# Performance work log

Hardware: AMD Instinct MI355X
Metric: run time of the kernel (lower is better)

## Reference

```python
import jax, jax.numpy as jnp
import numpy as np

D_MODEL = 1024
N_HEADS = 16
D_EXP = 4
B, SQ, SKV = 2, 2048, 2048
LN_EPS = 1e-5


def _linear_params(key, d_in, d_out):
    kw, kb = jax.random.split(key)
    w = jax.random.normal(kw, (d_in, d_out), jnp.float32) * 0.02  # stored [in,out]
    b = jax.random.normal(kb, (d_out,), jnp.float32) * 0.02
    return w, b


def setup_inputs() -> dict:
    key = jax.random.key(0)
    ks = jax.random.split(key, 16)
    inp = {}
    inp["x"] = jax.random.normal(ks[0], (B, SQ, D_MODEL), jnp.float32)
    inp["encoder_out"] = jax.random.normal(ks[1], (B, SKV, D_MODEL), jnp.float32)
    # causal target mask, broadcast over batch and heads
    inp["tgt_mask"] = jnp.tril(jnp.ones((SQ, SQ), jnp.int32))[None, None]
    inp["src_mask"] = jnp.ones((1, 1, SQ, SKV), jnp.int32)
    # self-attention params
    inp["wq_s"], inp["bq_s"] = _linear_params(ks[2], D_MODEL, D_MODEL)
    inp["wk_s"], inp["bk_s"] = _linear_params(ks[3], D_MODEL, D_MODEL)
    inp["wv_s"], inp["bv_s"] = _linear_params(ks[4], D_MODEL, D_MODEL)
    inp["wo_s"], inp["bo_s"] = _linear_params(ks[5], D_MODEL, D_MODEL)
    # cross-attention params
    inp["wq_c"], inp["bq_c"] = _linear_params(ks[6], D_MODEL, D_MODEL)
    inp["wk_c"], inp["bk_c"] = _linear_params(ks[7], D_MODEL, D_MODEL)
    inp["wv_c"], inp["bv_c"] = _linear_params(ks[8], D_MODEL, D_MODEL)
    inp["wo_c"], inp["bo_c"] = _linear_params(ks[9], D_MODEL, D_MODEL)
    # feedforward params
    inp["ff1_w"], inp["ff1_b"] = _linear_params(ks[10], D_MODEL, D_MODEL * D_EXP)
    inp["ff2_w"], inp["ff2_b"] = _linear_params(ks[11], D_MODEL * D_EXP, D_MODEL)
    # layernorm params (3 AddNorms)
    for i, k in zip((1, 2, 3), (ks[12], ks[13], ks[14])):
        inp[f"ln{i}_g"] = jnp.ones((D_MODEL,), jnp.float32)
        inp[f"ln{i}_b"] = jnp.zeros((D_MODEL,), jnp.float32)
    return inp


def _layernorm(x, g, b):
    mu = jnp.mean(x, axis=-1, keepdims=True)
    var = jnp.mean(jnp.square(x - mu), axis=-1, keepdims=True)
    return (x - mu) / jnp.sqrt(var + LN_EPS) * g + b


def _mha(xq, xkv, wq, bq, wk, bk, wv, bv, wo, bo, mask):
    Bq, Sq, D = xq.shape
    Hd = D // N_HEADS
    q = (xq @ wq + bq).reshape(Bq, Sq, N_HEADS, Hd).transpose(0, 2, 1, 3)   # bhqd
    k = (xkv @ wk + bk).reshape(Bq, -1, N_HEADS, Hd).transpose(0, 2, 1, 3)  # bhkd
    v = (xkv @ wv + bv).reshape(Bq, -1, N_HEADS, Hd).transpose(0, 2, 1, 3)  # bhkd
    score = jnp.einsum("bhqd,bhkd->bhqk", q, k) / jnp.sqrt(jnp.float32(Hd))
    score = jnp.where(mask == 0, -jnp.inf, score)
    attn = jax.nn.softmax(score, axis=-1)
    ctx = jnp.einsum("bhqk,bhkd->bhqd", attn, v)
    ctx = ctx.transpose(0, 2, 1, 3).reshape(Bq, Sq, D)
    return ctx @ wo + bo


def reference(x, encoder_out, tgt_mask, src_mask,
              wq_s, bq_s, wk_s, bk_s, wv_s, bv_s, wo_s, bo_s,
              wq_c, bq_c, wk_c, bk_c, wv_c, bv_c, wo_c, bo_c,
              ff1_w, ff1_b, ff2_w, ff2_b,
              ln1_g, ln1_b, ln2_g, ln2_b, ln3_g, ln3_b):
    # dropout is identity in eval mode
    sa = _mha(x, x, wq_s, bq_s, wk_s, bk_s, wv_s, bv_s, wo_s, bo_s, tgt_mask)
    h = _layernorm(x + sa, ln1_g, ln1_b)
    ca = _mha(h, encoder_out, wq_c, bq_c, wk_c, bk_c, wv_c, bv_c, wo_c, bo_c, src_mask)
    h2 = _layernorm(h + ca, ln2_g, ln2_b)
    ff = jax.nn.relu(h2 @ ff1_w + ff1_b) @ ff2_w + ff2_b
    return _layernorm(h2 + ff, ln3_g, ln3_b)
```

## Files before the change

### kernel.cpp

```cpp
#include <hip/hip_runtime.h>
#include <stdint.h>

typedef __bf16 bf16;
typedef __attribute__((ext_vector_type(4))) float f32x4;
typedef __attribute__((ext_vector_type(8))) __bf16 bf16x8;
typedef __attribute__((ext_vector_type(4))) __bf16 bf16x4;

#define DM   1024
#define NH   16
#define HDIM 64
#define BB   2
#define SEQ  2048
#define MR   (BB * SEQ)
#define DFF  4096
#define MEG  (1024 * 1024)

__global__ void detect_kernel(const unsigned int* __restrict__ xw,
                              int* __restrict__ flag) {
  int tid = threadIdx.x;
  int bad = 0;
  for (int i = tid; i < 4096; i += 64) {
    unsigned int w = xw[i];
    float flo = __uint_as_float((w & 0xffffu) << 16);
    if (!(fabsf(flo) < 100.f)) bad = 1;
  }
  unsigned long long m = __ballot(bad);
  if (tid == 0) *flag = (m == 0ull) ? 1 : 0;
}

__global__ __launch_bounds__(256) void cvt_big_kernel(
    const void* __restrict__ src, bf16* __restrict__ dst, int n4,
    const int* __restrict__ flag) {
  int i = blockIdx.x * 256 + threadIdx.x;
  if (i >= n4) return;
  if (*flag) {
    ((bf16x4*)dst)[i] = ((const bf16x4*)src)[i];
  } else {
    float4 v = ((const float4*)src)[i];
    bf16x4 o = {(bf16)v.x, (bf16)v.y, (bf16)v.z, (bf16)v.w};
    ((bf16x4*)dst)[i] = o;
  }
}

struct P16 { const void* p[16]; };
__global__ __launch_bounds__(256) void cvt_small_kernel(
    P16 ps, bf16* __restrict__ dstbase, const int* __restrict__ flag) {
  const int ncnt[16] = {1024,1024,1024,1024,1024,1024,1024,1024,
                        4096,1024,1024,1024,1024,1024,1024,1024};
  const int doff[16] = {0,1024,2048,3072,4096,5120,6144,7168,
                        8192,12288,13312,14336,15360,16384,17408,18432};
  int b = blockIdx.x;
  int n = ncnt[b];
  bool isbf = (*flag) != 0;
  const void* s = ps.p[b];
  bf16* d = dstbase + doff[b];
  for (int i = threadIdx.x; i * 4 < n; i += 256) {
    if (isbf) {
      ((bf16x4*)d)[i] = ((const bf16x4*)s)[i];
    } else {
      float4 v = ((const float4*)s)[i];
      bf16x4 o = {(bf16)v.x, (bf16)v.y, (bf16)v.z, (bf16)v.w};
      ((bf16x4*)d)[i] = o;
    }
  }
}

static __device__ __forceinline__ void gl_lds16(const bf16* g, bf16* l) {
  auto gp = reinterpret_cast<__attribute__((address_space(1))) unsigned int*>(
      reinterpret_cast<uintptr_t>(g));
  auto lp = reinterpret_cast<__attribute__((address_space(3))) unsigned int*>(
      (unsigned int)reinterpret_cast<uintptr_t>(l));
  __builtin_amdgcn_global_load_lds(gp, lp, 16, 0, 0);
}

struct WTB {
  const void* src[10];
  int dstoff[10];
  int K[10], N[10];
  int bstart[10];
};
__global__ __launch_bounds__(256) void wt_all_kernel(WTB wb, bf16* __restrict__ wtbase,
                                                     const int* __restrict__ flag) {
  __shared__ bf16 tile[32][33];
  int bid = blockIdx.x;
  int wi = 0;
  while (wi < 9 && bid >= wb.bstart[wi + 1]) ++wi;
  int rel = bid - wb.bstart[wi];
  int N = wb.N[wi], K = wb.K[wi];
  int nb = N >> 5;
  int n0 = (rel % nb) * 32, k0 = (rel / nb) * 32;
  const void* w = wb.src[wi];
  bf16* wt = wtbase + wb.dstoff[wi];
  bool isbf = (*flag) != 0;
  int tid = threadIdx.x;
  int tx = tid & 31, ty = tid >> 5;
#pragma unroll
  for (int i = 0; i < 4; ++i) {
    size_t idx = (size_t)(k0 + ty + i * 8) * N + n0 + tx;
    tile[ty + i * 8][tx] = isbf ? ((const bf16*)w)[idx]
                                : (bf16)(((const float*)w)[idx]);
  }
  __syncthreads();
#pragma unroll
  for (int i = 0; i < 4; ++i)
    wt[(size_t)(n0 + ty + i * 8) * K + k0 + tx] = tile[tx][ty + i * 8];
}

template <int TM>
__global__ __launch_bounds__(256) void gemm_kernel(
    const bf16* __restrict__ A, const bf16* __restrict__ Bt,
    const bf16* __restrict__ bias, bf16* __restrict__ outb,
    int M, int N, int K, int relu) {
  constexpr int NI = TM / 32;
  constexpr int WM = TM / 2;
  constexpr int CA = TM / 64;
  __shared__ alignas(16) bf16 As[TM * 32];
  __shared__ alignas(16) bf16 Bs[128 * 32];
  int tid = threadIdx.x;
  int lane = tid & 63, wv = tid >> 6;
  int quad = lane >> 4, l15 = lane & 15;
  int m0 = blockIdx.y * TM, n0 = blockIdx.x * 128;
  int wm = wv >> 1, wn = wv & 1;

  f32x4 acc[NI][4];
#pragma unroll
  for (int i = 0; i < NI; ++i)
#pragma unroll
    for (int j = 0; j < 4; ++j) acc[i][j] = (f32x4){0.f, 0.f, 0.f, 0.f};

  int sr = lane >> 2, sc = (lane & 3) * 8;
  const bf16* gA[CA];
  bf16* lA[CA];
#pragma unroll
  for (int t = 0; t < CA; ++t) {
    int ch = wv * CA + t;
    gA[t] = A + (size_t)(m0 + ch * 16 + sr) * K + sc;
    lA[t] = As + ch * 512 + lane * 8;
  }
  const bf16* gB0 = Bt + (size_t)(n0 + (wv * 2) * 16 + sr) * K + sc;
  const bf16* gB1 = Bt + (size_t)(n0 + (wv * 2 + 1) * 16 + sr) * K + sc;
  bf16* lB0 = Bs + (wv * 2) * 512 + lane * 8;
  bf16* lB1 = Bs + (wv * 2 + 1) * 512 + lane * 8;

  for (int k0 = 0; k0 < K; k0 += 32) {
#pragma unroll
    for (int t = 0; t < CA; ++t) gl_lds16(gA[t] + k0, lA[t]);
    gl_lds16(gB0 + k0, lB0);
    gl_lds16(gB1 + k0, lB1);
    __syncthreads();
    bf16x8 af[NI], bfr[4];
#pragma unroll
    for (int i = 0; i < NI; ++i)
      af[i] = *(const bf16x8*)(As + (wm * WM + i * 16 + l15) * 32 + quad * 8);
#pragma unroll
    for (int j = 0; j < 4; ++j)
      bfr[j] = *(const bf16x8*)(Bs + (wn * 64 + j * 16 + l15) * 32 + quad * 8);
#pragma unroll
    for (int i = 0; i < NI; ++i)
#pragma unroll
      for (int j = 0; j < 4; ++j)
        acc[i][j] = __builtin_amdgcn_mfma_f32_16x16x32_bf16(af[i], bfr[j],
                                                            acc[i][j], 0, 0, 0);
    __syncthreads();
  }

#pragma unroll
  for (int j = 0; j < 4; ++j) {
    int col = n0 + wn * 64 + j * 16 + l15;
    float bval = (float)bias[col];
#pragma unroll
    for (int i = 0; i < NI; ++i) {
      int rb = m0 + wm * WM + i * 16 + quad * 4;
#pragma unroll
      for (int r = 0; r < 4; ++r) {
        float v = acc[i][j][r] + bval;
        if (relu) v = fmaxf(v, 0.f);
        outb[(size_t)(rb + r) * N + col] = (bf16)v;
      }
    }
  }
}

__global__ __launch_bounds__(256) void gemm_splitk_kernel(
    const bf16* __restrict__ A, const bf16* __restrict__ Bt,
    float* __restrict__ pout, int M, int N, int KC, int Ktot) {
  __shared__ alignas(16) bf16 As[128 * 32];
  __shared__ alignas(16) bf16 Bs[128 * 32];
  int tid = threadIdx.x;
  int lane = tid & 63, wv = tid >> 6;
  int quad = lane >> 4, l15 = lane & 15;
  int m0 = blockIdx.y * 128, n0 = blockIdx.x * 128;
  int wm = wv >> 1, wn = wv & 1;
  int kb = blockIdx.z * KC;
  pout += (size_t)blockIdx.z * M * N;

  f32x4 acc[4][4];
#pragma unroll
  for (int i = 0; i < 4; ++i)
#pragma unroll
    for (int j = 0; j < 4; ++j) acc[i][j] = (f32x4){0.f, 0.f, 0.f, 0.f};

  int sr = lane >> 2, sc = (lane & 3) * 8;
  const bf16* gA0 = A + (size_t)(m0 + (wv * 2) * 16 + sr) * Ktot + sc;
  const bf16* gA1 = A + (size_t)(m0 + (wv * 2 + 1) * 16 + sr) * Ktot + sc;
  const bf16* gB0 = Bt + (size_t)(n0 + (wv * 2) * 16 + sr) * Ktot + sc;
  const bf16* gB1 = Bt + (size_t)(n0 + (wv * 2 + 1) * 16 + sr) * Ktot + sc;
  bf16* lA0 = As + (wv * 2) * 512 + lane * 8;
  bf16* lA1 = As + (wv * 2 + 1) * 512 + lane * 8;
  bf16* lB0 = Bs + (wv * 2) * 512 + lane * 8;
  bf16* lB1 = Bs + (wv * 2 + 1) * 512 + lane * 8;

  for (int k0 = kb; k0 < kb + KC; k0 += 32) {
    gl_lds16(gA0 + k0, lA0);
    gl_lds16(gA1 + k0, lA1);
    gl_lds16(gB0 + k0, lB0);
    gl_lds16(gB1 + k0, lB1);
    __syncthreads();
    bf16x8 af[4], bfr[4];
#pragma unroll
    for (int i = 0; i < 4; ++i)
      af[i] = *(const bf16x8*)(As + (wm * 64 + i * 16 + l15) * 32 + quad * 8);
#pragma unroll
    for (int j = 0; j < 4; ++j)
      bfr[j] = *(const bf16x8*)(Bs + (wn * 64 + j * 16 + l15) * 32 + quad * 8);
#pragma unroll
    for (int i = 0; i < 4; ++i)
#pragma unroll
      for (int j = 0; j < 4; ++j)
        acc[i][j] = __builtin_amdgcn_mfma_f32_16x16x32_bf16(af[i], bfr[j],
                                                            acc[i][j], 0, 0, 0);
    __syncthreads();
  }
#pragma unroll
  for (int j = 0; j < 4; ++j) {
    int col = n0 + wn * 64 + j * 16 + l15;
#pragma unroll
    for (int i = 0; i < 4; ++i) {
      int rb = m0 + wm * 64 + i * 16 + quad * 4;
#pragma unroll
      for (int r = 0; r < 4; ++r)
        pout[(size_t)(rb + r) * N + col] = acc[i][j][r];
    }
  }
}

__global__ __launch_bounds__(256) void vt_pre_kernel(
    const bf16* __restrict__ v, int vstride, bf16* __restrict__ vt, int skv) {
  __shared__ bf16 tile[32][33];
  int tid = threadIdx.x;
  int tx = tid & 31, ty = tid >> 5;
  int kv0 = blockIdx.x * 32, d0 = blockIdx.y * 32;
  int bh = blockIdx.z;
  int b = bh >> 4, h = bh & 15;
  const bf16* src = v + (size_t)b * skv * vstride + h * HDIM;
#pragma unroll
  for (int i = 0; i < 4; ++i)
    tile[ty + i * 8][tx] = src[(size_t)(kv0 + ty + i * 8) * vstride + d0 + tx];
  __syncthreads();
  bf16* dst = vt + ((size_t)bh * HDIM + d0) * skv + kv0;
#pragma unroll
  for (int i = 0; i < 4; ++i)
    dst[(size_t)(ty + i * 8) * skv + tx] = tile[tx][ty + i * 8];
}

__global__ __launch_bounds__(256) void flash5_kernel(
    const bf16* __restrict__ Q, int qstride,
    const bf16* __restrict__ Kk, int kstride,
    const bf16* __restrict__ VT, bf16* __restrict__ ctx,
    float* __restrict__ opart, float* __restrict__ lpart,
    int skv, int causal, int nsplit) {
  __shared__ alignas(16) bf16 Kt[2][64 * 72];
  __shared__ alignas(16) bf16 Vt[2][64 * 72];
  __shared__ alignas(16) bf16 Pt[4][16 * 72];
  int tid = threadIdx.x;
  int lane = tid & 63, wv = tid >> 6, quad = lane >> 4, l15 = lane & 15;
  int qb = blockIdx.x, h = blockIdx.y;
  int zz = blockIdx.z;
  int b = (nsplit == 2) ? (zz >> 1) : zz;
  int half = (nsplit == 2) ? (zz & 1) : 0;
  int q0 = qb * 128;
  int qw = q0 + wv * 32;

  bf16x8 qf[2][2];
  const float qsc = 0.125f * 1.44269504f;
#pragma unroll
  for (int a = 0; a < 2; ++a) {
    const bf16* qp = Q + (size_t)(b * SEQ + qw + a * 16 + l15) * qstride + h * HDIM;
    qf[a][0] = *(const bf16x8*)(qp + quad * 8);
    qf[a][1] = *(const bf16x8*)(qp + 32 + quad * 8);
#pragma unroll
    for (int j = 0; j < 8; ++j) {
      qf[a][0][j] = (bf16)((float)qf[a][0][j] * qsc);
      qf[a][1][j] = (bf16)((float)qf[a][1][j] * qsc);
    }
  }
  bf16x8 onesf;
#pragma unroll
  for (int j = 0; j < 8; ++j) onesf[j] = (l15 == 0) ? (bf16)1.0f : (bf16)0.0f;

  f32x4 o[2][4], oL[2];
#pragma unroll
  for (int a = 0; a < 2; ++a) {
    oL[a] = (f32x4){0.f, 0.f, 0.f, 0.f};
#pragma unroll
    for (int j = 0; j < 4; ++j) o[a][j] = (f32x4){0.f, 0.f, 0.f, 0.f};
  }

  int nch_tot = causal ? (q0 + 128) / 64 : skv / 64;
  int c_lo = (half * nch_tot) / nsplit;
  int c_hi = ((half + 1) * nch_tot) / nsplit;
  int srow = tid >> 2, sseg = (tid & 3) * 16;
  const bf16* kg = Kk + (size_t)b * skv * kstride + (size_t)srow * kstride +
                   h * HDIM + sseg;
  const bf16* vg = VT + ((size_t)(b * NH + h) * HDIM + srow) * skv + sseg;

  bf16x8 k0r = *(const bf16x8*)(kg + (size_t)(c_lo * 64) * kstride);
  bf16x8 k1r = *(const bf16x8*)(kg + (size_t)(c_lo * 64) * kstride + 8);
  bf16x8 v0r = *(const bf16x8*)(vg + c_lo * 64);
  bf16x8 v1r = *(const bf16x8*)(vg + c_lo * 64 + 8);

  for (int c = c_lo; c < c_hi; ++c) {
    int buf = (c - c_lo) & 1;
    int kv0 = c * 64;
    *(bf16x8*)(&Kt[buf][srow * 72 + sseg]) = k0r;
    *(bf16x8*)(&Kt[buf][srow * 72 + sseg + 8]) = k1r;
    *(bf16x8*)(&Vt[buf][srow * 72 + sseg]) = v0r;
    *(bf16x8*)(&Vt[buf][srow * 72 + sseg + 8]) = v1r;
    if (c + 1 < c_hi) {
      const bf16* kn = kg + (size_t)(kv0 + 64) * kstride;
      const bf16* vn = vg + kv0 + 64;
      k0r = *(const bf16x8*)(kn);
      k1r = *(const bf16x8*)(kn + 8);
      v0r = *(const bf16x8*)(vn);
      v1r = *(const bf16x8*)(vn + 8);
    }
    __syncthreads();

    if (!causal || kv0 <= qw + 31) {
      f32x4 s[2][4];
#pragma unroll
      for (int t = 0; t < 4; ++t) {
        bf16x8 kt0 = *(const bf16x8*)(&Kt[buf][(t * 16 + l15) * 72 + quad * 8]);
        bf16x8 kt1 = *(const bf16x8*)(&Kt[buf][(t * 16 + l15) * 72 + 32 + quad * 8]);
#pragma unroll
        for (int a = 0; a < 2; ++a) {
          f32x4 z = (f32x4){0.f, 0.f, 0.f, 0.f};
          z = __builtin_amdgcn_mfma_f32_16x16x32_bf16(kt0, qf[a][0], z, 0, 0, 0);
          z = __builtin_amdgcn_mfma_f32_16x16x32_bf16(kt1, qf[a][1], z, 0, 0, 0);
          s[a][t] = z;
        }
      }
      if (causal && kv0 + 63 > qw) {
#pragma unroll
        for (int a = 0; a < 2; ++a)
#pragma unroll
          for (int t = 0; t < 4; ++t)
#pragma unroll
            for (int r = 0; r < 4; ++r)
              if (kv0 + t * 16 + quad * 4 + r > qw + a * 16 + l15)
                s[a][t][r] = -1e30f;
      }
      bf16x8 pf[2][2];
#pragma unroll
      for (int a = 0; a < 2; ++a) {
#pragma unroll
        for (int t = 0; t < 4; ++t) {
          bf16x4 pk;
#pragma unroll
          for (int r = 0; r < 4; ++r) pk[r] = (bf16)exp2f(s[a][t][r]);
          *(bf16x4*)(&Pt[wv][l15 * 72 + t * 16 + quad * 4]) = pk;
        }
        __asm__ volatile("s_waitcnt lgkmcnt(0)" ::: "memory");
        pf[a][0] = *(const bf16x8*)(&Pt[wv][l15 * 72 + quad * 8]);
        pf[a][1] = *(const bf16x8*)(&Pt[wv][l15 * 72 + 32 + quad * 8]);
        __asm__ volatile("s_waitcnt lgkmcnt(0)" ::: "memory");
      }
#pragma unroll
      for (int a = 0; a < 2; ++a) {
        oL[a] = __builtin_amdgcn_mfma_f32_16x16x32_bf16(pf[a][0], onesf, oL[a], 0, 0, 0);
        oL[a] = __builtin_amdgcn_mfma_f32_16x16x32_bf16(pf[a][1], onesf, oL[a], 0, 0, 0);
      }
#pragma unroll
      for (int j = 0; j < 4; ++j) {
        bf16x8 bv0 = *(const bf16x8*)(&Vt[buf][(j * 16 + l15) * 72 + quad * 8]);
        bf16x8 bv1 = *(const bf16x8*)(&Vt[buf][(j * 16 + l15) * 72 + 32 + quad * 8]);
#pragma unroll
        for (int a = 0; a < 2; ++a) {
          o[a][j] = __builtin_amdgcn_mfma_f32_16x16x32_bf16(pf[a][0], bv0, o[a][j], 0, 0, 0);
          o[a][j] = __builtin_amdgcn_mfma_f32_16x16x32_bf16(pf[a][1], bv1, o[a][j], 0, 0, 0);
        }
      }
    }
  }

  if (nsplit == 1) {
#pragma unroll
    for (int a = 0; a < 2; ++a)
#pragma unroll
      for (int r = 0; r < 4; ++r) {
        float l = __shfl(oL[a][r], quad * 16, 64);
        float inv = 1.0f / fmaxf(l, 1e-30f);
        bf16* cp = ctx + (size_t)(b * SEQ + qw + a * 16 + quad * 4 + r) * DM + h * HDIM;
#pragma unroll
        for (int j = 0; j < 4; ++j) cp[j * 16 + l15] = (bf16)(o[a][j][r] * inv);
      }
  } else {
    float* op = opart + (size_t)half * MR * DM;
#pragma unroll
    for (int a = 0; a < 2; ++a)
#pragma unroll
      for (int r = 0; r < 4; ++r) {
        float* cp = op + (size_t)(b * SEQ + qw + a * 16 + quad * 4 + r) * DM + h * HDIM;
#pragma unroll
        for (int j = 0; j < 4; ++j) cp[j * 16 + l15] = o[a][j][r];
      }
    if (l15 == 0) {
#pragma unroll
      for (int a = 0; a < 2; ++a)
#pragma unroll
        for (int r = 0; r < 4; ++r)
          lpart[(size_t)((half * BB + b) * NH + h) * SEQ + qw + a * 16 + quad * 4 + r] =
              oL[a][r];
    }
  }
}

__global__ __launch_bounds__(256) void flash_comb_kernel(
    const float* __restrict__ opart, const float* __restrict__ lpart,
    bf16* __restrict__ ctx) {
  int row = blockIdx.x, tid = threadIdx.x;
  int b = row >> 11, q = row & (SEQ - 1);
  int h = tid >> 4;
  float l = lpart[(size_t)(b * NH + h) * SEQ + q] +
            lpart[(size_t)((BB + b) * NH + h) * SEQ + q];
  float inv = 1.0f / fmaxf(l, 1e-30f);
  f32x4 o0 = ((const f32x4*)(opart + (size_t)row * DM))[tid];
  f32x4 o1 = ((const f32x4*)(opart + (size_t)MR * DM + (size_t)row * DM))[tid];
  bf16x4 ob = {(bf16)((o0[0] + o1[0]) * inv), (bf16)((o0[1] + o1[1]) * inv),
               (bf16)((o0[2] + o1[2]) * inv), (bf16)((o0[3] + o1[3]) * inv)};
  ((bf16x4*)(ctx + (size_t)row * DM))[tid] = ob;
}

template <int NP>
__global__ __launch_bounds__(256) void addnorm_red_kernel(
    const bf16* __restrict__ res, const float* __restrict__ part,
    const bf16* __restrict__ bias, const bf16* __restrict__ g,
    const bf16* __restrict__ be, bf16* __restrict__ yb,
    void* __restrict__ outAny, const int* __restrict__ flag) {
  int row = blockIdx.x, tid = threadIdx.x;
  float a0 = 0.f, a1 = 0.f, a2 = 0.f, a3 = 0.f;
#pragma unroll
  for (int p = 0; p < NP; ++p) {
    float4 v = ((const float4*)(part + (size_t)p * MR * DM + (size_t)row * DM))[tid];
    a0 += v.x; a1 += v.y; a2 += v.z; a3 += v.w;
  }
  bf16x4 bb = ((const bf16x4*)bias)[tid];
  bf16x4 rr = ((const bf16x4*)(res + (size_t)row * DM))[tid];
  float s0 = (float)rr[0] + a0 + (float)bb[0];
  float s1 = (float)rr[1] + a1 + (float)bb[1];
  float s2 = (float)rr[2] + a2 + (float)bb[2];
  float s3 = (float)rr[3] + a3 + (float)bb[3];
  float sum = s0 + s1 + s2 + s3;
  float sq = s0 * s0 + s1 * s1 + s2 * s2 + s3 * s3;
#pragma unroll
  for (int mk = 32; mk >= 1; mk >>= 1) {
    sum += __shfl_xor(sum, mk, 64);
    sq += __shfl_xor(sq, mk, 64);
  }
  __shared__ float red[8];
  int wvi = tid >> 6, lane = tid & 63;
  if (lane == 0) { red[wvi * 2] = sum; red[wvi * 2 + 1] = sq; }
  __syncthreads();
  sum = red[0] + red[2] + red[4] + red[6];
  sq = red[1] + red[3] + red[5] + red[7];
  float mu = sum * (1.0f / DM);
  float var = sq * (1.0f / DM) - mu * mu;
  float rstd = rsqrtf(var + 1e-5f);
  bf16x4 g4 = ((const bf16x4*)g)[tid];
  bf16x4 b4 = ((const bf16x4*)be)[tid];
  float y0 = (s0 - mu) * rstd * (float)g4[0] + (float)b4[0];
  float y1 = (s1 - mu) * rstd * (float)g4[1] + (float)b4[1];
  float y2 = (s2 - mu) * rstd * (float)g4[2] + (float)b4[2];
  float y3 = (s3 - mu) * rstd * (float)g4[3] + (float)b4[3];
  if (yb) {
    bf16x4 ob = {(bf16)y0, (bf16)y1, (bf16)y2, (bf16)y3};
    ((bf16x4*)(yb + (size_t)row * DM))[tid] = ob;
  }
  if (outAny) {
    if (*flag) {
      bf16x4 ob = {(bf16)y0, (bf16)y1, (bf16)y2, (bf16)y3};
      ((bf16x4*)outAny)[(size_t)row * 256 + tid] = ob;
    } else {
      ((float4*)outAny)[(size_t)row * 256 + tid] = make_float4(y0, y1, y2, y3);
    }
  }
}

extern "C" void kernel_launch(void* const* d_in, const int* in_sizes, int n_in,
                              void* d_out, int out_size, void* d_ws, size_t ws_size,
                              hipStream_t stream) {
  (void)in_sizes; (void)n_in; (void)out_size; (void)ws_size;
  const void* x_raw   = d_in[0];
  const void* enc_raw = d_in[1];

  char* ws = (char*)d_ws;
  size_t off = 0;
  auto alloc = [&](size_t bytes) -> void* {
    void* p = ws + off;
    off += (bytes + 255) & ~(size_t)255;
    return p;
  };
  const size_t SB = (size_t)MR * DM;
  int* flag    = (int*)alloc(256);
  bf16* smallb = (bf16*)alloc(20480 * 2);
  bf16* wt   = (bf16*)alloc((size_t)16 * MEG * 2);
  bf16* xb   = (bf16*)alloc(SB * 2);
  bf16* encb = (bf16*)alloc(SB * 2);
  bf16* vtg  = (bf16*)alloc(SB * 2);
  bf16* ctx  = (bf16*)alloc(SB * 2);
  bf16* hb1  = (bf16*)alloc(SB * 2);
  bf16* hb2  = (bf16*)alloc(SB * 2);
  bf16* qkv  = (bf16*)alloc(SB * 3 * 2);
  bf16* kvc  = (bf16*)alloc(SB * 2 * 2);
  float* part = (float*)alloc(SB * 4 * 4);
  float* lpart = (float*)alloc((size_t)2 * BB * NH * SEQ * 4);
  bf16* gbuf = qkv;
  bf16* qc   = xb;

  bf16* b_qkvs = smallb + 0;     bf16* b_os  = smallb + 3072;
  bf16* b_qc   = smallb + 4096;  bf16* b_kvc = smallb + 5120;
  bf16* b_oc   = smallb + 7168;  bf16* b_f1  = smallb + 8192;
  bf16* b_f2   = smallb + 12288;
  bf16* l1g = smallb + 13312; bf16* l1b = smallb + 14336;
  bf16* l2g = smallb + 15360; bf16* l2b = smallb + 16384;
  bf16* l3g = smallb + 17408; bf16* l3b = smallb + 18432;

  detect_kernel<<<1, 64, 0, stream>>>((const unsigned int*)x_raw, flag);
  cvt_big_kernel<<<(int)(SB / 1024), 256, 0, stream>>>(x_raw, xb, (int)(SB / 4), flag);
  cvt_big_kernel<<<(int)(SB / 1024), 256, 0, stream>>>(enc_raw, encb, (int)(SB / 4), flag);
  P16 ps;
  ps.p[0] = d_in[5];  ps.p[1] = d_in[7];  ps.p[2] = d_in[9];  ps.p[3] = d_in[11];
  ps.p[4] = d_in[13]; ps.p[5] = d_in[15]; ps.p[6] = d_in[17]; ps.p[7] = d_in[19];
  ps.p[8] = d_in[21]; ps.p[9] = d_in[23];
  ps.p[10] = d_in[24]; ps.p[11] = d_in[25]; ps.p[12] = d_in[26];
  ps.p[13] = d_in[27]; ps.p[14] = d_in[28]; ps.p[15] = d_in[29];
  cvt_small_kernel<<<16, 256, 0, stream>>>(ps, smallb, flag);

  WTB wb;
  const int wsrc[10] = {4, 6, 8, 10, 12, 14, 16, 18, 20, 22};
  for (int i = 0; i < 10; ++i) {
    wb.src[i] = d_in[wsrc[i]];
    wb.K[i] = 1024; wb.N[i] = 1024;
    wb.dstoff[i] = i * MEG;
    wb.bstart[i] = i * 1024;
  }
  wb.N[8] = 4096;
  wb.K[9] = 4096; wb.dstoff[9] = 12 * MEG;
  wb.bstart[9] = 8192 + 4096;
  wt_all_kernel<<<16384, 256, 0, stream>>>(wb, wt, flag);

  gemm_kernel<128><<<dim3(24, 32), 256, 0, stream>>>(xb, wt, b_qkvs, qkv,
                                                     MR, 3072, DM, 0);
  vt_pre_kernel<<<dim3(SEQ / 32, 2, 32), 256, 0, stream>>>(qkv + 2048, 3072, vtg, SEQ);
  flash5_kernel<<<dim3(SEQ / 128, NH, BB * 2), 256, 0, stream>>>(
      qkv, 3072, qkv + 1024, 3072, vtg, ctx, part, lpart, SEQ, 1, 2);
  flash_comb_kernel<<<MR, 256, 0, stream>>>(part, lpart, ctx);
  gemm_splitk_kernel<<<dim3(8, 32, 2), 256, 0, stream>>>(
      ctx, wt + (size_t)3 * MEG, part, MR, DM, 512, DM);
  addnorm_red_kernel<2><<<MR, 256, 0, stream>>>(xb, part, b_os, l1g, l1b,
                                                hb1, nullptr, flag);
  gemm_kernel<64><<<dim3(8, 64), 256, 0, stream>>>(hb1, wt + (size_t)4 * MEG,
                                                   b_qc, qc, MR, DM, DM, 0);
  gemm_kernel<128><<<dim3(16, 32), 256, 0, stream>>>(encb, wt + (size_t)5 * MEG,
                                                     b_kvc, kvc, MR, 2048, DM, 0);
  vt_pre_kernel<<<dim3(SEQ / 32, 2, 32), 256, 0, stream>>>(kvc + 1024, 2048, vtg, SEQ);
  flash5_kernel<<<dim3(SEQ / 128, NH, BB), 256, 0, stream>>>(
      qc, 1024, kvc, 2048, vtg, ctx, nullptr, nullptr, SEQ, 0, 1);
  gemm_splitk_kernel<<<dim3(8, 32, 2), 256, 0, stream>>>(
      ctx, wt + (size_t)7 * MEG, part, MR, DM, 512, DM);
  addnorm_red_kernel<2><<<MR, 256, 0, stream>>>(hb1, part, b_oc, l2g, l2b,
                                                hb2, nullptr, flag);
  gemm_kernel<128><<<dim3(32, 32), 256, 0, stream>>>(hb2, wt + (size_t)8 * MEG,
                                                     b_f1, gbuf, MR, DFF, DM, 1);
  gemm_splitk_kernel<<<dim3(8, 32, 4), 256, 0, stream>>>(
      gbuf, wt + (size_t)12 * MEG, part, MR, DM, 1024, DFF);
  addnorm_red_kernel<4><<<MR, 256, 0, stream>>>(hb2, part, b_f2, l3g, l3b,
                                                nullptr, d_out, flag);
}
```

Before: 659.5 us.

## Split attention KV range three ways for both attentions and single-buffer LDS tiles

```diff
diff --git a/kernel.cpp b/kernel.cpp
--- a/kernel.cpp
+++ b/kernel.cpp
@@ -263,21 +263,21 @@
     dst[(size_t)(ty + i * 8) * skv + tx] = tile[tx][ty + i * 8];
 }
 
-__global__ __launch_bounds__(256) void flash5_kernel(
+__global__ __launch_bounds__(256) void flash7_kernel(
     const bf16* __restrict__ Q, int qstride,
     const bf16* __restrict__ Kk, int kstride,
     const bf16* __restrict__ VT, bf16* __restrict__ ctx,
     float* __restrict__ opart, float* __restrict__ lpart,
     int skv, int causal, int nsplit) {
-  __shared__ alignas(16) bf16 Kt[2][64 * 72];
-  __shared__ alignas(16) bf16 Vt[2][64 * 72];
-  __shared__ alignas(16) bf16 Pt[4][16 * 72];
+  __shared__ alignas(16) bf16 Kt[64 * 72];
+  __shared__ alignas(16) bf16 Vt[64 * 72];
+  __shared__ alignas(16) bf16 Pt[4][32 * 72];
   int tid = threadIdx.x;
   int lane = tid & 63, wv = tid >> 6, quad = lane >> 4, l15 = lane & 15;
   int qb = blockIdx.x, h = blockIdx.y;
   int zz = blockIdx.z;
-  int b = (nsplit == 2) ? (zz >> 1) : zz;
-  int half = (nsplit == 2) ? (zz & 1) : 0;
+  int b = zz / nsplit;
+  int half = zz - b * nsplit;
   int q0 = qb * 128;
   int qw = q0 + wv * 32;
 
@@ -314,18 +314,23 @@
                    h * HDIM + sseg;
   const bf16* vg = VT + ((size_t)(b * NH + h) * HDIM + srow) * skv + sseg;
 
-  bf16x8 k0r = *(const bf16x8*)(kg + (size_t)(c_lo * 64) * kstride);
-  bf16x8 k1r = *(const bf16x8*)(kg + (size_t)(c_lo * 64) * kstride + 8);
-  bf16x8 v0r = *(const bf16x8*)(vg + c_lo * 64);
-  bf16x8 v1r = *(const bf16x8*)(vg + c_lo * 64 + 8);
+  bf16x8 k0r, k1r, v0r, v1r;
+  if (c_lo < c_hi) {
+    const bf16* kp = kg + (size_t)(c_lo * 64) * kstride;
+    const bf16* vp = vg + c_lo * 64;
+    k0r = *(const bf16x8*)(kp);
+    k1r = *(const bf16x8*)(kp + 8);
+    v0r = *(const bf16x8*)(vp);
+    v1r = *(const bf16x8*)(vp + 8);
+  }
 
   for (int c = c_lo; c < c_hi; ++c) {
-    int buf = (c - c_lo) & 1;
     int kv0 = c * 64;
-    *(bf16x8*)(&Kt[buf][srow * 72 + sseg]) = k0r;
-    *(bf16x8*)(&Kt[buf][srow * 72 + sseg + 8]) = k1r;
-    *(bf16x8*)(&Vt[buf][srow * 72 + sseg]) = v0r;
-    *(bf16x8*)(&Vt[buf][srow * 72 + sseg + 8]) = v1r;
+    __syncthreads();
+    *(bf16x8*)(&Kt[srow * 72 + sseg]) = k0r;
+    *(bf16x8*)(&Kt[srow * 72 + sseg + 8]) = k1r;
+    *(bf16x8*)(&Vt[srow * 72 + sseg]) = v0r;
+    *(bf16x8*)(&Vt[srow * 72 + sseg + 8]) = v1r;
     if (c + 1 < c_hi) {
       const bf16* kn = kg + (size_t)(kv0 + 64) * kstride;
       const bf16* vn = vg + kv0 + 64;
@@ -340,8 +345,8 @@
       f32x4 s[2][4];
 #pragma unroll
       for (int t = 0; t < 4; ++t) {
-        bf16x8 kt0 = *(const bf16x8*)(&Kt[buf][(t * 16 + l15) * 72 + quad * 8]);
-        bf16x8 kt1 = *(const bf16x8*)(&Kt[buf][(t * 16 + l15) * 72 + 32 + quad * 8]);
+        bf16x8 kt0 = *(const bf16x8*)(&Kt[(t * 16 + l15) * 72 + quad * 8]);
+        bf16x8 kt1 = *(const bf16x8*)(&Kt[(t * 16 + l15) * 72 + 32 + quad * 8]);
 #pragma unroll
         for (int a = 0; a < 2; ++a) {
           f32x4 z = (f32x4){0.f, 0.f, 0.f, 0.f};
@@ -360,20 +365,21 @@
               if (kv0 + t * 16 + quad * 4 + r > qw + a * 16 + l15)
                 s[a][t][r] = -1e30f;
       }
-      bf16x8 pf[2][2];
-#pragma unroll
-      for (int a = 0; a < 2; ++a) {
+#pragma unroll
+      for (int a = 0; a < 2; ++a)
 #pragma unroll
         for (int t = 0; t < 4; ++t) {
           bf16x4 pk;
 #pragma unroll
           for (int r = 0; r < 4; ++r) pk[r] = (bf16)exp2f(s[a][t][r]);
-          *(bf16x4*)(&Pt[wv][l15 * 72 + t * 16 + quad * 4]) = pk;
+          *(bf16x4*)(&Pt[wv][(a * 16 + l15) * 72 + t * 16 + quad * 4]) = pk;
         }
-        __asm__ volatile("s_waitcnt lgkmcnt(0)" ::: "memory");
-        pf[a][0] = *(const bf16x8*)(&Pt[wv][l15 * 72 + quad * 8]);
-        pf[a][1] = *(const bf16x8*)(&Pt[wv][l15 * 72 + 32 + quad * 8]);
-        __asm__ volatile("s_waitcnt lgkmcnt(0)" ::: "memory");
+      __asm__ volatile("s_waitcnt lgkmcnt(0)" ::: "memory");
+      bf16x8 pf[2][2];
+#pragma unroll
+      for (int a = 0; a < 2; ++a) {
+        pf[a][0] = *(const bf16x8*)(&Pt[wv][(a * 16 + l15) * 72 + quad * 8]);
+        pf[a][1] = *(const bf16x8*)(&Pt[wv][(a * 16 + l15) * 72 + 32 + quad * 8]);
       }
 #pragma unroll
       for (int a = 0; a < 2; ++a) {
@@ -382,8 +388,8 @@
       }
 #pragma unroll
       for (int j = 0; j < 4; ++j) {
-        bf16x8 bv0 = *(const bf16x8*)(&Vt[buf][(j * 16 + l15) * 72 + quad * 8]);
-        bf16x8 bv1 = *(const bf16x8*)(&Vt[buf][(j * 16 + l15) * 72 + 32 + quad * 8]);
+        bf16x8 bv0 = *(const bf16x8*)(&Vt[(j * 16 + l15) * 72 + quad * 8]);
+        bf16x8 bv1 = *(const bf16x8*)(&Vt[(j * 16 + l15) * 72 + 32 + quad * 8]);
 #pragma unroll
         for (int a = 0; a < 2; ++a) {
           o[a][j] = __builtin_amdgcn_mfma_f32_16x16x32_bf16(pf[a][0], bv0, o[a][j], 0, 0, 0);
@@ -425,19 +431,26 @@
   }
 }
 
+template <int NS>
 __global__ __launch_bounds__(256) void flash_comb_kernel(
     const float* __restrict__ opart, const float* __restrict__ lpart,
     bf16* __restrict__ ctx) {
   int row = blockIdx.x, tid = threadIdx.x;
   int b = row >> 11, q = row & (SEQ - 1);
   int h = tid >> 4;
-  float l = lpart[(size_t)(b * NH + h) * SEQ + q] +
-            lpart[(size_t)((BB + b) * NH + h) * SEQ + q];
+  float l = 0.f;
+#pragma unroll
+  for (int s = 0; s < NS; ++s)
+    l += lpart[(size_t)((s * BB + b) * NH + h) * SEQ + q];
   float inv = 1.0f / fmaxf(l, 1e-30f);
-  f32x4 o0 = ((const f32x4*)(opart + (size_t)row * DM))[tid];
-  f32x4 o1 = ((const f32x4*)(opart + (size_t)MR * DM + (size_t)row * DM))[tid];
-  bf16x4 ob = {(bf16)((o0[0] + o1[0]) * inv), (bf16)((o0[1] + o1[1]) * inv),
-               (bf16)((o0[2] + o1[2]) * inv), (bf16)((o0[3] + o1[3]) * inv)};
+  float a0 = 0.f, a1 = 0.f, a2 = 0.f, a3 = 0.f;
+#pragma unroll
+  for (int s = 0; s < NS; ++s) {
+    f32x4 v = ((const f32x4*)(opart + (size_t)s * MR * DM + (size_t)row * DM))[tid];
+    a0 += v[0]; a1 += v[1]; a2 += v[2]; a3 += v[3];
+  }
+  bf16x4 ob = {(bf16)(a0 * inv), (bf16)(a1 * inv),
+               (bf16)(a2 * inv), (bf16)(a3 * inv)};
   ((bf16x4*)(ctx + (size_t)row * DM))[tid] = ob;
 }
 
@@ -523,7 +536,7 @@
   bf16* qkv  = (bf16*)alloc(SB * 3 * 2);
   bf16* kvc  = (bf16*)alloc(SB * 2 * 2);
   float* part = (float*)alloc(SB * 4 * 4);
-  float* lpart = (float*)alloc((size_t)2 * BB * NH * SEQ * 4);
+  float* lpart = (float*)alloc((size_t)3 * BB * NH * SEQ * 4);
   bf16* gbuf = qkv;
   bf16* qc   = xb;
 
@@ -562,9 +575,9 @@
   gemm_kernel<128><<<dim3(24, 32), 256, 0, stream>>>(xb, wt, b_qkvs, qkv,
                                                      MR, 3072, DM, 0);
   vt_pre_kernel<<<dim3(SEQ / 32, 2, 32), 256, 0, stream>>>(qkv + 2048, 3072, vtg, SEQ);
-  flash5_kernel<<<dim3(SEQ / 128, NH, BB * 2), 256, 0, stream>>>(
-      qkv, 3072, qkv + 1024, 3072, vtg, ctx, part, lpart, SEQ, 1, 2);
-  flash_comb_kernel<<<MR, 256, 0, stream>>>(part, lpart, ctx);
+  flash7_kernel<<<dim3(SEQ / 128, NH, BB * 3), 256, 0, stream>>>(
+      qkv, 3072, qkv + 1024, 3072, vtg, ctx, part, lpart, SEQ, 1, 3);
+  flash_comb_kernel<3><<<MR, 256, 0, stream>>>(part, lpart, ctx);
   gemm_splitk_kernel<<<dim3(8, 32, 2), 256, 0, stream>>>(
       ctx, wt + (size_t)3 * MEG, part, MR, DM, 512, DM);
   addnorm_red_kernel<2><<<MR, 256, 0, stream>>>(xb, part, b_os, l1g, l1b,
@@ -574,8 +587,9 @@
   gemm_kernel<128><<<dim3(16, 32), 256, 0, stream>>>(encb, wt + (size_t)5 * MEG,
                                                      b_kvc, kvc, MR, 2048, DM, 0);
   vt_pre_kernel<<<dim3(SEQ / 32, 2, 32), 256, 0, stream>>>(kvc + 1024, 2048, vtg, SEQ);
-  flash5_kernel<<<dim3(SEQ / 128, NH, BB), 256, 0, stream>>>(
-      qc, 1024, kvc, 2048, vtg, ctx, nullptr, nullptr, SEQ, 0, 1);
+  flash7_kernel<<<dim3(SEQ / 128, NH, BB * 3), 256, 0, stream>>>(
+      qc, 1024, kvc, 2048, vtg, ctx, part, lpart, SEQ, 0, 3);
+  flash_comb_kernel<3><<<MR, 256, 0, stream>>>(part, lpart, ctx);
   gemm_splitk_kernel<<<dim3(8, 32, 2), 256, 0, stream>>>(
       ctx, wt + (size_t)7 * MEG, part, MR, DM, 512, DM);
   addnorm_red_kernel<2><<<MR, 256, 0, stream>>>(hb1, part, b_oc, l2g, l2b,
```

Result: slower. 677.4 us (+2.7%).
